# Kernel tuning notes

Hardware: AMD Instinct MI355X
Metric: run time of the kernel (lower is better)

Reference implementation:

```python
import jax, jax.numpy as jnp
import numpy as np

DIM = 2048
SEQ = 8192
NUM_HEADS = 16
PROJ_DIM = DIM // 4  # proj_ratio = 4.0
EPS = 1e-5


def setup_inputs() -> dict:
    key = jax.random.key(0)
    ks = jax.random.split(key, 8)
    s = 0.02  # param init scale
    return {
        "x": jax.random.normal(ks[0], (SEQ, DIM), jnp.float32),
        "q": jax.random.normal(ks[1], (1, DIM), jnp.float32),
        "W_kv": jax.random.normal(ks[2], (2 * DIM, DIM), jnp.float32) * s,
        "b_kv": jax.random.normal(ks[3], (2 * DIM,), jnp.float32) * s,
        "W_p1": jax.random.normal(ks[4], (PROJ_DIM, DIM), jnp.float32) * s,
        "b_p1": jax.random.normal(ks[5], (PROJ_DIM,), jnp.float32) * s,
        "W_p2": jax.random.normal(ks[6], (DIM, PROJ_DIM), jnp.float32) * s,
        "b_p2": jax.random.normal(ks[7], (DIM,), jnp.float32) * s,
        "ln_w": jnp.ones((PROJ_DIM,), jnp.float32),
        "ln_b": jnp.zeros((PROJ_DIM,), jnp.float32),
    }


def reference(x, q, W_kv, b_kv, W_p1, b_p1, W_p2, b_p2, ln_w, ln_b):
    seq, dim = x.shape
    h = NUM_HEADS
    d = dim // h

    # kv projection: [s, 2*dim]; split '(n h d)' with n leading -> k = first dim cols
    kv = x @ W_kv.T + b_kv
    k = kv[:, :dim].reshape(seq, h, d).transpose(1, 0, 2)   # [h, s, d]
    v = kv[:, dim:].reshape(seq, h, d).transpose(1, 0, 2)   # [h, s, d]
    qh = q.reshape(h, 1, d)                                  # '1 (h d) -> h 1 d'

    # single-query attention (qk_norm=False -> Identity norms)
    attn = jnp.einsum('hqd,hkd->hqk', qh, k) / jnp.sqrt(jnp.asarray(d, x.dtype))
    attn = jax.nn.softmax(attn, axis=-1)                     # [h, 1, s]
    x1 = jnp.einsum('hqk,hkd->hqd', attn, v)                 # [h, 1, d]
    x1 = x1.transpose(1, 0, 2).reshape(1, dim)               # 'h s d -> s (h d)'

    # proj MLP: proj1 -> LayerNorm -> relu -> proj2
    h1 = x1 @ W_p1.T + b_p1                                  # [1, proj_dim]
    mu = jnp.mean(h1, axis=-1, keepdims=True)
    var = jnp.mean(jnp.square(h1 - mu), axis=-1, keepdims=True)
    h1 = (h1 - mu) / jnp.sqrt(var + EPS) * ln_w + ln_b
    x1 = jax.nn.relu(h1) @ W_p2.T + b_p2                     # [1, dim]

    # residual broadcast: [s, dim] + [1, dim]
    return x + x1
```

## Files before the change

kernel.cpp:

```cpp
#include <hip/hip_runtime.h>
#include <math.h>

#define SEQ   8192
#define DIM   2048
#define NH    16
#define DH    128
#define PD    512

static constexpr float LN_EPS = 1e-5f;
static constexpr float SCALE  = 0.08838834764831845f;

typedef __bf16 bf16x8 __attribute__((ext_vector_type(8)));
typedef float  f32x4  __attribute__((ext_vector_type(4)));

static constexpr size_t OFF_QB   = 0;
static constexpr size_t OFF_SMP  = 16;
static constexpr size_t OFF_QWB  = 528;
static constexpr size_t OFF_ELOG = OFF_QWB + 16384;
static constexpr size_t OFF_PCTX = OFF_ELOG + 131072;
static constexpr size_t OFF_CTX  = OFF_PCTX + 128*32768;
static constexpr size_t OFF_X1   = OFF_CTX + 32768;
static constexpr size_t OFF_H1R  = OFF_X1 + 2048;
static constexpr size_t OFF_X1F  = OFF_H1R + 512;

__global__ __launch_bounds__(256) void k_prep(const float* __restrict__ q,
                                              const float* __restrict__ Wkv,
                                              const float* __restrict__ bkv,
                                              __bf16* __restrict__ qWb,
                                              float* __restrict__ qb,
                                              float* __restrict__ smp) {
    int t = threadIdx.x;
    int h = blockIdx.x >> 4, jc = blockIdx.x & 15;
    int col = t & 127, kh = t >> 7;
    int j = jc * 128 + col;
    const float* w  = Wkv + (size_t)(h * DH + kh * 64) * DIM + j;
    const float* qh = q + h * DH + kh * 64;
    float acc = 0.f;
#pragma unroll 16
    for (int d = 0; d < 64; ++d)
        acc += qh[d] * w[(size_t)d * DIM];
    __shared__ float part[128];
    if (kh) part[col] = acc;
    __syncthreads();
    if (!kh) qWb[h * DIM + j] = (__bf16)(acc + part[col]);
    if (jc == 0 && t < 64) {
        float p = q[h*DH + t] * bkv[h*DH + t] + q[h*DH + 64 + t] * bkv[h*DH + 64 + t];
        for (int off = 32; off; off >>= 1) p += __shfl_down(p, off);
        if (t == 0) qb[h] = p;
    }
    if (blockIdx.x == 0) { smp[t] = 0.f; smp[t + 256] = 0.f; }
}

__global__ __launch_bounds__(256) void k_logits(const float* __restrict__ x,
                                                const __bf16* __restrict__ qWb,
                                                const float* __restrict__ qb,
                                                float* __restrict__ elogT,
                                                float* __restrict__ smp) {
    const int t = threadIdx.x;
    const int w = t >> 6, lane = t & 63;
    const int r = lane & 15, quad = lane >> 4;
    const int s0 = blockIdx.x * 16;
    __shared__ float dpart[4][64][4];
    __shared__ float hsum[NH];
    if (t < NH) hsum[t] = 0.f;

    const float*  xrow = x + (size_t)(s0 + r) * DIM + quad * 8;
    const __bf16* brow = qWb + r * DIM + quad * 8;
    const int kbase = w * 512;

    f32x4 acc = {0.f, 0.f, 0.f, 0.f};
#pragma unroll 4
    for (int i = 0; i < 16; ++i) {
        int k = kbase + i * 32;
        float4 xa = *(const float4*)(xrow + k);
        float4 xb = *(const float4*)(xrow + k + 4);
        bf16x8 af;
        af[0] = (__bf16)xa.x; af[1] = (__bf16)xa.y;
        af[2] = (__bf16)xa.z; af[3] = (__bf16)xa.w;
        af[4] = (__bf16)xb.x; af[5] = (__bf16)xb.y;
        af[6] = (__bf16)xb.z; af[7] = (__bf16)xb.w;
        bf16x8 bf = *(const bf16x8*)(brow + k);
        acc = __builtin_amdgcn_mfma_f32_16x16x32_bf16(af, bf, acc, 0, 0, 0);
    }
    dpart[w][lane][0] = acc[0];
    dpart[w][lane][1] = acc[1];
    dpart[w][lane][2] = acc[2];
    dpart[w][lane][3] = acc[3];
    __syncthreads();

    {
        const int lane2 = t & 63, reg = t >> 6;
        const int h = lane2 & 15, sl = (lane2 >> 4) * 4 + reg;
        float v = dpart[0][lane2][reg] + dpart[1][lane2][reg]
                + dpart[2][lane2][reg] + dpart[3][lane2][reg];
        float e = __expf((v + qb[h]) * SCALE);
        elogT[(size_t)(s0 + sl) * NH + h] = e;
        atomicAdd(&hsum[h], e);
    }
    __syncthreads();
    if (t < NH) atomicAdd(&smp[t * 32 + (blockIdx.x & 31)], hsum[t]);
}

__global__ __launch_bounds__(256) void k_ctx(const float* __restrict__ x,
                                             const float* __restrict__ elogT,
                                             const float* __restrict__ smp,
                                             float* __restrict__ pctx) {
    int jc = blockIdx.x & 3, sc = blockIdx.x >> 2, t = threadIdx.x;
    int s0 = sc * 64;
    int j = jc * 512 + t * 2;
    __shared__ float inv_s[NH];
    __shared__ float att[64][NH];
    if (t < NH) {
        float S = 0.f;
#pragma unroll
        for (int i = 0; i < 32; ++i) S += smp[t * 32 + i];
        inv_s[t] = 1.0f / S;
    }
    __syncthreads();
    for (int i = t; i < 64 * NH; i += 256) {
        int rr = i >> 4, h = i & 15;
        att[rr][h] = elogT[(size_t)(s0 + rr) * NH + h] * inv_s[h];
    }
    __syncthreads();
    float2 acc[NH];
#pragma unroll
    for (int h = 0; h < NH; ++h) acc[h] = make_float2(0.f, 0.f);
    for (int rr = 0; rr < 64; ++rr) {
        float2 xv = *(const float2*)&x[(size_t)(s0 + rr) * DIM + j];
        const float4* ar = (const float4*)att[rr];
        float4 a0 = ar[0], a1 = ar[1], a2 = ar[2], a3 = ar[3];
        float aa[NH];
        *(float4*)&aa[0] = a0; *(float4*)&aa[4]  = a1;
        *(float4*)&aa[8] = a2; *(float4*)&aa[12] = a3;
#pragma unroll
        for (int h = 0; h < NH; ++h) {
            acc[h].x += aa[h] * xv.x;
            acc[h].y += aa[h] * xv.y;
        }
    }
#pragma unroll
    for (int h = 0; h < NH; ++h)
        *(float2*)&pctx[((size_t)(sc * NH + h)) * DIM + j] = acc[h];
}

__global__ __launch_bounds__(256) void k_ctxred(const float* __restrict__ pctx,
                                                float* __restrict__ ctx) {
    int idx = blockIdx.x * 256 + threadIdx.x;
    float s = 0.f;
#pragma unroll 8
    for (int sc = 0; sc < 128; ++sc)
        s += pctx[(size_t)sc * (NH * DIM) + idx];
    ctx[idx] = s;
}

__global__ __launch_bounds__(256) void k_x1(const float* __restrict__ Wkv,
                                            const float* __restrict__ bkv,
                                            const float* __restrict__ ctx,
                                            float* __restrict__ x1) {
    int row = blockIdx.x * 4 + (threadIdx.x >> 6);
    int lane = threadIdx.x & 63;
    const float* w = Wkv + (size_t)(DIM + row) * DIM;
    const float* c = ctx + (row >> 7) * DIM;
    float acc = 0.f;
#pragma unroll
    for (int k = 0; k < 8; ++k) {
        int j = k * 256 + lane * 4;
        float4 wv = *(const float4*)&w[j];
        float4 cv = *(const float4*)&c[j];
        acc += wv.x*cv.x + wv.y*cv.y + wv.z*cv.z + wv.w*cv.w;
    }
    for (int off = 32; off; off >>= 1) acc += __shfl_xor(acc, off);
    if (lane == 0) x1[row] = acc + bkv[DIM + row];
}

__global__ __launch_bounds__(256) void k_h1(const float* __restrict__ Wp1,
                                            const float* __restrict__ bp1,
                                            const float* __restrict__ x1,
                                            float* __restrict__ h1raw) {
    int row = blockIdx.x * 4 + (threadIdx.x >> 6);
    int lane = threadIdx.x & 63;
    const float* w = Wp1 + (size_t)row * DIM;
    float acc = 0.f;
#pragma unroll
    for (int k = 0; k < 8; ++k) {
        int j = k * 256 + lane * 4;
        float4 wv = *(const float4*)&w[j];
        float4 cv = *(const float4*)&x1[j];
        acc += wv.x*cv.x + wv.y*cv.y + wv.z*cv.z + wv.w*cv.w;
    }
    for (int off = 32; off; off >>= 1) acc += __shfl_xor(acc, off);
    if (lane == 0) h1raw[row] = acc + bp1[row];
}

__global__ __launch_bounds__(256) void k_x1f(const float* __restrict__ Wp2,
                                             const float* __restrict__ bp2,
                                             const float* __restrict__ h1raw,
                                             const float* __restrict__ lnw,
                                             const float* __restrict__ lnb,
                                             float* __restrict__ x1f) {
    int row = blockIdx.x * 4 + (threadIdx.x >> 6);
    int lane = threadIdx.x & 63;
    int j = lane * 8;
    float4 va = *(const float4*)&h1raw[j];
    float4 vb = *(const float4*)&h1raw[j + 4];
    float s = va.x + va.y + va.z + va.w + vb.x + vb.y + vb.z + vb.w;
    for (int off = 32; off; off >>= 1) s += __shfl_xor(s, off);
    float mu = s * (1.0f / PD);
    float dx[8];
    dx[0]=va.x-mu; dx[1]=va.y-mu; dx[2]=va.z-mu; dx[3]=va.w-mu;
    dx[4]=vb.x-mu; dx[5]=vb.y-mu; dx[6]=vb.z-mu; dx[7]=vb.w-mu;
    float s2 = 0.f;
#pragma unroll
    for (int i = 0; i < 8; ++i) s2 += dx[i] * dx[i];
    for (int off = 32; off; off >>= 1) s2 += __shfl_xor(s2, off);
    float rstd = rsqrtf(s2 * (1.0f / PD) + LN_EPS);
    float4 lw0 = *(const float4*)&lnw[j], lw1 = *(const float4*)&lnw[j + 4];
    float4 lb0 = *(const float4*)&lnb[j], lb1 = *(const float4*)&lnb[j + 4];
    float hln[8];
    hln[0]=fmaxf(dx[0]*rstd*lw0.x+lb0.x,0.f); hln[1]=fmaxf(dx[1]*rstd*lw0.y+lb0.y,0.f);
    hln[2]=fmaxf(dx[2]*rstd*lw0.z+lb0.z,0.f); hln[3]=fmaxf(dx[3]*rstd*lw0.w+lb0.w,0.f);
    hln[4]=fmaxf(dx[4]*rstd*lw1.x+lb1.x,0.f); hln[5]=fmaxf(dx[5]*rstd*lw1.y+lb1.y,0.f);
    hln[6]=fmaxf(dx[6]*rstd*lw1.z+lb1.z,0.f); hln[7]=fmaxf(dx[7]*rstd*lw1.w+lb1.w,0.f);
    const float* w = Wp2 + (size_t)row * PD + j;
    float4 w0 = *(const float4*)w, w1 = *(const float4*)(w + 4);
    float acc = w0.x*hln[0] + w0.y*hln[1] + w0.z*hln[2] + w0.w*hln[3]
              + w1.x*hln[4] + w1.y*hln[5] + w1.z*hln[6] + w1.w*hln[7];
    for (int off = 32; off; off >>= 1) acc += __shfl_xor(acc, off);
    if (lane == 0) x1f[row] = acc + bp2[row];
}

__global__ __launch_bounds__(256) void k_out(const float* __restrict__ x,
                                             const float* __restrict__ x1f,
                                             float* __restrict__ out) {
    size_t i = (size_t)blockIdx.x * 512 + threadIdx.x;
    float4 xv = ((const float4*)x)[i];
    float4 a  = ((const float4*)x1f)[(int)(i & 511)];
    ((float4*)out)[i] = make_float4(xv.x + a.x, xv.y + a.y, xv.z + a.z, xv.w + a.w);
    size_t i2 = i + 256;
    float4 xv2 = ((const float4*)x)[i2];
    float4 a2  = ((const float4*)x1f)[(int)(i2 & 511)];
    ((float4*)out)[i2] = make_float4(xv2.x + a2.x, xv2.y + a2.y, xv2.z + a2.z, xv2.w + a2.w);
}

extern "C" void kernel_launch(void* const* d_in, const int* in_sizes, int n_in,
                              void* d_out, int out_size, void* d_ws, size_t ws_size,
                              hipStream_t stream) {
    const float* x    = (const float*)d_in[0];
    const float* q    = (const float*)d_in[1];
    const float* Wkv  = (const float*)d_in[2];
    const float* bkv  = (const float*)d_in[3];
    const float* Wp1  = (const float*)d_in[4];
    const float* bp1  = (const float*)d_in[5];
    const float* Wp2  = (const float*)d_in[6];
    const float* bp2  = (const float*)d_in[7];
    const float* lnw  = (const float*)d_in[8];
    const float* lnb  = (const float*)d_in[9];
    float* out = (float*)d_out;
    float* ws  = (float*)d_ws;

    float*  qb    = ws + OFF_QB;
    float*  smp   = ws + OFF_SMP;
    __bf16* qWb   = (__bf16*)(ws + OFF_QWB);
    float*  elogT = ws + OFF_ELOG;
    float*  pctx  = ws + OFF_PCTX;
    float*  ctx   = ws + OFF_CTX;
    float*  x1    = ws + OFF_X1;
    float*  h1raw = ws + OFF_H1R;
    float*  x1f   = ws + OFF_X1F;

    k_prep  <<<256, 256, 0, stream>>>(q, Wkv, bkv, qWb, qb, smp);
    k_logits<<<512, 256, 0, stream>>>(x, qWb, qb, elogT, smp);
    k_ctx   <<<512, 256, 0, stream>>>(x, elogT, smp, pctx);
    k_ctxred<<<128, 256, 0, stream>>>(pctx, ctx);
    k_x1    <<<512, 256, 0, stream>>>(Wkv, bkv, ctx, x1);
    k_h1    <<<128, 256, 0, stream>>>(Wp1, bp1, x1, h1raw);
    k_x1f   <<<512, 256, 0, stream>>>(Wp2, bp2, h1raw, lnw, lnb, x1f);
    k_out   <<<8192, 256, 0, stream>>>(x, x1f, out);
}
```

Measured before the change: 223.7 us.

## Fuse logits and context accumulation into one kernel with deferred softmax normalization

Merges the logit kernel and the weighted-context kernel so each block of 32 rows computes the exp-logits into shared memory and immediately accumulates the attention-weighted sum of x, so x is read only once per tile. Softmax normalization moves into the reduction kernel, and the elogT workspace round-trip goes away. The partial-context buffer doubles to 256 chunks, which adds reduction traffic. Nontemporal loads and stores are also applied to the weight streams and the output write.

```diff
diff --git a/kernel.cpp b/kernel.cpp
--- a/kernel.cpp
+++ b/kernel.cpp
@@ -16,9 +16,8 @@
 static constexpr size_t OFF_QB   = 0;
 static constexpr size_t OFF_SMP  = 16;
 static constexpr size_t OFF_QWB  = 528;
-static constexpr size_t OFF_ELOG = OFF_QWB + 16384;
-static constexpr size_t OFF_PCTX = OFF_ELOG + 131072;
-static constexpr size_t OFF_CTX  = OFF_PCTX + 128*32768;
+static constexpr size_t OFF_PCTX = 16912;
+static constexpr size_t OFF_CTX  = OFF_PCTX + 8388608;
 static constexpr size_t OFF_X1   = OFF_CTX + 32768;
 static constexpr size_t OFF_H1R  = OFF_X1 + 2048;
 static constexpr size_t OFF_X1F  = OFF_H1R + 512;
@@ -38,7 +37,7 @@
     float acc = 0.f;
 #pragma unroll 16
     for (int d = 0; d < 64; ++d)
-        acc += qh[d] * w[(size_t)d * DIM];
+        acc += qh[d] * __builtin_nontemporal_load(w + (size_t)d * DIM);
     __shared__ float part[128];
     if (kh) part[col] = acc;
     __syncthreads();
@@ -51,106 +50,96 @@
     if (blockIdx.x == 0) { smp[t] = 0.f; smp[t + 256] = 0.f; }
 }
 
-__global__ __launch_bounds__(256) void k_logits(const float* __restrict__ x,
-                                                const __bf16* __restrict__ qWb,
-                                                const float* __restrict__ qb,
-                                                float* __restrict__ elogT,
-                                                float* __restrict__ smp) {
-    const int t = threadIdx.x;
-    const int w = t >> 6, lane = t & 63;
+__global__ __launch_bounds__(512) void k_fctx(const float* __restrict__ x,
+                                              const __bf16* __restrict__ qWb,
+                                              const float* __restrict__ qb,
+                                              float* __restrict__ pctx,
+                                              float* __restrict__ smp) {
+    const int b = blockIdx.x, t = threadIdx.x;
+    const int w8 = t >> 6, lane = t & 63;
+    const int s0 = b * 32;
+    const int rg = w8 & 1, kq = w8 >> 1;
     const int r = lane & 15, quad = lane >> 4;
-    const int s0 = blockIdx.x * 16;
-    __shared__ float dpart[4][64][4];
+
+    __shared__ float dpart[2][4][64][4];
+    __shared__ float att[32][NH];
     __shared__ float hsum[NH];
     if (t < NH) hsum[t] = 0.f;
 
-    const float*  xrow = x + (size_t)(s0 + r) * DIM + quad * 8;
+    const float*  xrow = x + (size_t)(s0 + rg * 16 + r) * DIM + quad * 8;
     const __bf16* brow = qWb + r * DIM + quad * 8;
-    const int kbase = w * 512;
-
+    const int kbase = kq * 512;
     f32x4 acc = {0.f, 0.f, 0.f, 0.f};
 #pragma unroll 4
     for (int i = 0; i < 16; ++i) {
         int k = kbase + i * 32;
-        float4 xa = *(const float4*)(xrow + k);
-        float4 xb = *(const float4*)(xrow + k + 4);
+        float4 xa  = *(const float4*)(xrow + k);
+        float4 xb2 = *(const float4*)(xrow + k + 4);
         bf16x8 af;
-        af[0] = (__bf16)xa.x; af[1] = (__bf16)xa.y;
-        af[2] = (__bf16)xa.z; af[3] = (__bf16)xa.w;
-        af[4] = (__bf16)xb.x; af[5] = (__bf16)xb.y;
-        af[6] = (__bf16)xb.z; af[7] = (__bf16)xb.w;
-        bf16x8 bf = *(const bf16x8*)(brow + k);
-        acc = __builtin_amdgcn_mfma_f32_16x16x32_bf16(af, bf, acc, 0, 0, 0);
-    }
-    dpart[w][lane][0] = acc[0];
-    dpart[w][lane][1] = acc[1];
-    dpart[w][lane][2] = acc[2];
-    dpart[w][lane][3] = acc[3];
+        af[0] = (__bf16)xa.x;  af[1] = (__bf16)xa.y;
+        af[2] = (__bf16)xa.z;  af[3] = (__bf16)xa.w;
+        af[4] = (__bf16)xb2.x; af[5] = (__bf16)xb2.y;
+        af[6] = (__bf16)xb2.z; af[7] = (__bf16)xb2.w;
+        bf16x8 bfv = *(const bf16x8*)(brow + k);
+        acc = __builtin_amdgcn_mfma_f32_16x16x32_bf16(af, bfv, acc, 0, 0, 0);
+    }
+    *(f32x4*)&dpart[rg][kq][lane][0] = acc;
     __syncthreads();
 
     {
-        const int lane2 = t & 63, reg = t >> 6;
-        const int h = lane2 & 15, sl = (lane2 >> 4) * 4 + reg;
-        float v = dpart[0][lane2][reg] + dpart[1][lane2][reg]
-                + dpart[2][lane2][reg] + dpart[3][lane2][reg];
+        const int h = t & 15, slp = t >> 4;
+        const int rg2 = slp >> 4, sli = slp & 15;
+        const int quad2 = sli >> 2, reg2 = sli & 3;
+        const int lane2 = quad2 * 16 + h;
+        float v = dpart[rg2][0][lane2][reg2] + dpart[rg2][1][lane2][reg2]
+                + dpart[rg2][2][lane2][reg2] + dpart[rg2][3][lane2][reg2];
         float e = __expf((v + qb[h]) * SCALE);
-        elogT[(size_t)(s0 + sl) * NH + h] = e;
+        att[slp][h] = e;
         atomicAdd(&hsum[h], e);
     }
     __syncthreads();
-    if (t < NH) atomicAdd(&smp[t * 32 + (blockIdx.x & 31)], hsum[t]);
-}
-
-__global__ __launch_bounds__(256) void k_ctx(const float* __restrict__ x,
-                                             const float* __restrict__ elogT,
-                                             const float* __restrict__ smp,
-                                             float* __restrict__ pctx) {
-    int jc = blockIdx.x & 3, sc = blockIdx.x >> 2, t = threadIdx.x;
-    int s0 = sc * 64;
-    int j = jc * 512 + t * 2;
-    __shared__ float inv_s[NH];
-    __shared__ float att[64][NH];
-    if (t < NH) {
-        float S = 0.f;
-#pragma unroll
-        for (int i = 0; i < 32; ++i) S += smp[t * 32 + i];
-        inv_s[t] = 1.0f / S;
-    }
-    __syncthreads();
-    for (int i = t; i < 64 * NH; i += 256) {
-        int rr = i >> 4, h = i & 15;
-        att[rr][h] = elogT[(size_t)(s0 + rr) * NH + h] * inv_s[h];
-    }
-    __syncthreads();
-    float2 acc[NH];
-#pragma unroll
-    for (int h = 0; h < NH; ++h) acc[h] = make_float2(0.f, 0.f);
-    for (int rr = 0; rr < 64; ++rr) {
-        float2 xv = *(const float2*)&x[(size_t)(s0 + rr) * DIM + j];
-        const float4* ar = (const float4*)att[rr];
-        float4 a0 = ar[0], a1 = ar[1], a2 = ar[2], a3 = ar[3];
-        float aa[NH];
-        *(float4*)&aa[0] = a0; *(float4*)&aa[4]  = a1;
-        *(float4*)&aa[8] = a2; *(float4*)&aa[12] = a3;
-#pragma unroll
-        for (int h = 0; h < NH; ++h) {
-            acc[h].x += aa[h] * xv.x;
-            acc[h].y += aa[h] * xv.y;
-        }
+    if (t < NH) atomicAdd(&smp[t * 32 + (b & 31)], hsum[t]);
+
+    const int j0 = t * 4;
+    f32x4 zero = {0.f, 0.f, 0.f, 0.f};
+    f32x4 acc4[NH];
+#pragma unroll
+    for (int h = 0; h < NH; ++h) acc4[h] = zero;
+#pragma unroll 2
+    for (int rr = 0; rr < 32; ++rr) {
+        f32x4 xv = *(const f32x4*)(x + (size_t)(s0 + rr) * DIM + j0);
+        const f32x4* ar = (const f32x4*)att[rr];
+        f32x4 a0 = ar[0], a1 = ar[1], a2 = ar[2], a3 = ar[3];
+        float aa[16];
+        *(f32x4*)&aa[0] = a0; *(f32x4*)&aa[4]  = a1;
+        *(f32x4*)&aa[8] = a2; *(f32x4*)&aa[12] = a3;
+#pragma unroll
+        for (int h = 0; h < NH; ++h) acc4[h] += xv * aa[h];
     }
 #pragma unroll
     for (int h = 0; h < NH; ++h)
-        *(float2*)&pctx[((size_t)(sc * NH + h)) * DIM + j] = acc[h];
+        __builtin_nontemporal_store(acc4[h],
+            (f32x4*)&pctx[((size_t)(b * NH + h)) * DIM + j0]);
 }
 
 __global__ __launch_bounds__(256) void k_ctxred(const float* __restrict__ pctx,
+                                                const float* __restrict__ smp,
                                                 float* __restrict__ ctx) {
-    int idx = blockIdx.x * 256 + threadIdx.x;
+    const int b = blockIdx.x, t = threadIdx.x;
+    const int h = b >> 3;
+    __shared__ float sInv;
+    if (t < 32) {
+        float v = smp[h * 32 + t];
+        for (int off = 16; off; off >>= 1) v += __shfl_xor(v, off);
+        if (t == 0) sInv = 1.0f / v;
+    }
+    __syncthreads();
+    const size_t idx = (size_t)b * 256 + t;
     float s = 0.f;
 #pragma unroll 8
-    for (int sc = 0; sc < 128; ++sc)
-        s += pctx[(size_t)sc * (NH * DIM) + idx];
-    ctx[idx] = s;
+    for (int c = 0; c < 256; ++c)
+        s += __builtin_nontemporal_load(&pctx[(size_t)c * (NH * DIM) + idx]);
+    ctx[idx] = s * sInv;
 }
 
 __global__ __launch_bounds__(256) void k_x1(const float* __restrict__ Wkv,
@@ -165,9 +154,9 @@
 #pragma unroll
     for (int k = 0; k < 8; ++k) {
         int j = k * 256 + lane * 4;
-        float4 wv = *(const float4*)&w[j];
-        float4 cv = *(const float4*)&c[j];
-        acc += wv.x*cv.x + wv.y*cv.y + wv.z*cv.z + wv.w*cv.w;
+        f32x4 wv = __builtin_nontemporal_load((const f32x4*)&w[j]);
+        f32x4 cv = *(const f32x4*)&c[j];
+        acc += wv[0]*cv[0] + wv[1]*cv[1] + wv[2]*cv[2] + wv[3]*cv[3];
     }
     for (int off = 32; off; off >>= 1) acc += __shfl_xor(acc, off);
     if (lane == 0) x1[row] = acc + bkv[DIM + row];
@@ -184,9 +173,9 @@
 #pragma unroll
     for (int k = 0; k < 8; ++k) {
         int j = k * 256 + lane * 4;
-        float4 wv = *(const float4*)&w[j];
-        float4 cv = *(const float4*)&x1[j];
-        acc += wv.x*cv.x + wv.y*cv.y + wv.z*cv.z + wv.w*cv.w;
+        f32x4 wv = __builtin_nontemporal_load((const f32x4*)&w[j]);
+        f32x4 cv = *(const f32x4*)&x1[j];
+        acc += wv[0]*cv[0] + wv[1]*cv[1] + wv[2]*cv[2] + wv[3]*cv[3];
     }
     for (int off = 32; off; off >>= 1) acc += __shfl_xor(acc, off);
     if (lane == 0) h1raw[row] = acc + bp1[row];
@@ -222,9 +211,10 @@
     hln[4]=fmaxf(dx[4]*rstd*lw1.x+lb1.x,0.f); hln[5]=fmaxf(dx[5]*rstd*lw1.y+lb1.y,0.f);
     hln[6]=fmaxf(dx[6]*rstd*lw1.z+lb1.z,0.f); hln[7]=fmaxf(dx[7]*rstd*lw1.w+lb1.w,0.f);
     const float* w = Wp2 + (size_t)row * PD + j;
-    float4 w0 = *(const float4*)w, w1 = *(const float4*)(w + 4);
-    float acc = w0.x*hln[0] + w0.y*hln[1] + w0.z*hln[2] + w0.w*hln[3]
-              + w1.x*hln[4] + w1.y*hln[5] + w1.z*hln[6] + w1.w*hln[7];
+    f32x4 w0 = __builtin_nontemporal_load((const f32x4*)w);
+    f32x4 w1 = __builtin_nontemporal_load((const f32x4*)(w + 4));
+    float acc = w0[0]*hln[0] + w0[1]*hln[1] + w0[2]*hln[2] + w0[3]*hln[3]
+              + w1[0]*hln[4] + w1[1]*hln[5] + w1[2]*hln[6] + w1[3]*hln[7];
     for (int off = 32; off; off >>= 1) acc += __shfl_xor(acc, off);
     if (lane == 0) x1f[row] = acc + bp2[row];
 }
@@ -233,13 +223,13 @@
                                              const float* __restrict__ x1f,
                                              float* __restrict__ out) {
     size_t i = (size_t)blockIdx.x * 512 + threadIdx.x;
-    float4 xv = ((const float4*)x)[i];
-    float4 a  = ((const float4*)x1f)[(int)(i & 511)];
-    ((float4*)out)[i] = make_float4(xv.x + a.x, xv.y + a.y, xv.z + a.z, xv.w + a.w);
+    f32x4 xv = ((const f32x4*)x)[i];
+    f32x4 a  = ((const f32x4*)x1f)[(int)(i & 511)];
+    __builtin_nontemporal_store(xv + a, (f32x4*)out + i);
     size_t i2 = i + 256;
-    float4 xv2 = ((const float4*)x)[i2];
-    float4 a2  = ((const float4*)x1f)[(int)(i2 & 511)];
-    ((float4*)out)[i2] = make_float4(xv2.x + a2.x, xv2.y + a2.y, xv2.z + a2.z, xv2.w + a2.w);
+    f32x4 xv2 = ((const f32x4*)x)[i2];
+    f32x4 a2  = ((const f32x4*)x1f)[(int)(i2 & 511)];
+    __builtin_nontemporal_store(xv2 + a2, (f32x4*)out + i2);
 }
 
 extern "C" void kernel_launch(void* const* d_in, const int* in_sizes, int n_in,
@@ -261,7 +251,6 @@
     float*  qb    = ws + OFF_QB;
     float*  smp   = ws + OFF_SMP;
     __bf16* qWb   = (__bf16*)(ws + OFF_QWB);
-    float*  elogT = ws + OFF_ELOG;
     float*  pctx  = ws + OFF_PCTX;
     float*  ctx   = ws + OFF_CTX;
     float*  x1    = ws + OFF_X1;
@@ -269,9 +258,8 @@
     float*  x1f   = ws + OFF_X1F;
 
     k_prep  <<<256, 256, 0, stream>>>(q, Wkv, bkv, qWb, qb, smp);
-    k_logits<<<512, 256, 0, stream>>>(x, qWb, qb, elogT, smp);
-    k_ctx   <<<512, 256, 0, stream>>>(x, elogT, smp, pctx);
-    k_ctxred<<<128, 256, 0, stream>>>(pctx, ctx);
+    k_fctx  <<<256, 512, 0, stream>>>(x, qWb, qb, pctx, smp);
+    k_ctxred<<<128, 256, 0, stream>>>(pctx, smp, ctx);
     k_x1    <<<512, 256, 0, stream>>>(Wkv, bkv, ctx, x1);
     k_h1    <<<128, 256, 0, stream>>>(Wp1, bp1, x1, h1raw);
     k_x1f   <<<512, 256, 0, stream>>>(Wp2, bp2, h1raw, lnw, lnb, x1f);
```

Result: no change. 221.1 us (-1.2%).
